# Optimization experiments

Measured on AMD Instinct MI355X. Metric: run time of the kernel, lower is better.

Reference implementation:

```python
import jax, jax.numpy as jnp
import numpy as np

B, S, H, E = 2, 4096, 2048, 8


def setup_inputs() -> dict:
    key = jax.random.key(0)
    k1, k2, k3 = jax.random.split(key, 3)
    x = jax.random.normal(k1, (B, S, H), dtype=jnp.float32)
    w_router = jax.random.normal(k2, (E, H), dtype=jnp.float32) * (1.0 / np.sqrt(H))
    # nn.Linear weight layout: [out_features, in_features] per expert -> [E, H, H]
    w_experts = jax.random.normal(k3, (E, H, H), dtype=jnp.float32) * (1.0 / np.sqrt(H))
    return {"x": x, "w_router": w_router, "w_experts": w_experts}


def reference(x, w_router, w_experts):
    # router logits: x @ W_r^T  -> [B, S, E]
    logits = jnp.einsum('bsh,eh->bse', x, w_router)
    idx = jnp.argmax(logits, axis=-1)  # [B, S] top-1 expert per token
    # dense all-expert outputs (matches original which evaluates every expert):
    # expert_e(x) = x @ W_e^T -> [B, S, E, H]
    all_out = jnp.einsum('bsh,efh->bsef', x, w_experts)
    # masked sum over one-hot mask == gather of the selected expert output
    out = jnp.take_along_axis(all_out, idx[:, :, None, None], axis=2)[:, :, 0, :]
    return out
```

## Files before the change

kernel.cpp:

```cpp
#include <hip/hip_runtime.h>
#include <hip/hip_bf16.h>
#include <cstdint>

#define T_TOK 8192
#define H_DIM 2048
#define N_EXP 8
#define FLAGBIT 0x80000000u

typedef __attribute__((ext_vector_type(4))) float f32x4;
typedef __attribute__((ext_vector_type(8))) short bf16x8;

__device__ __forceinline__ unsigned short f2bf(float f) {
  unsigned int u = __builtin_bit_cast(unsigned int, f);
  u += 0x7fffu + ((u >> 16) & 1u);
  return (unsigned short)(u >> 16);
}

#define GLL(SRC, DST) __builtin_amdgcn_global_load_lds( \
    (const __attribute__((address_space(1))) void*)(SRC), \
    (__attribute__((address_space(3))) void*)(DST), 16, 0, 0)

__global__ __launch_bounds__(256, 2) void k_conv(const float* __restrict__ we,
                                                 unsigned short* __restrict__ wb) {
  const size_t tix = ((size_t)blockIdx.x * 256 + threadIdx.x) * 8;
  const size_t stride = (size_t)2048 * 256 * 8;
  f32x4 v[16];
#pragma unroll
  for (int it = 0; it < 8; ++it) {
    v[2 * it]     = *reinterpret_cast<const f32x4*>(we + tix + (size_t)it * stride);
    v[2 * it + 1] = *reinterpret_cast<const f32x4*>(we + tix + (size_t)it * stride + 4);
  }
#pragma unroll
  for (int q = 0; q < 16; ++q) asm volatile("" : "+v"(v[q]));
#pragma unroll
  for (int it = 0; it < 8; ++it) {
    union { unsigned short h[8]; uint4 u; } r;
#pragma unroll
    for (int q = 0; q < 4; ++q) {
      r.h[q]     = f2bf(v[2 * it][q]);
      r.h[4 + q] = f2bf(v[2 * it + 1][q]);
    }
    *reinterpret_cast<uint4*>(wb + tix + (size_t)it * stride) = r.u;
  }
}

__global__ __launch_bounds__(256) void k_router(const float* __restrict__ x,
    const float* __restrict__ wr, unsigned short* __restrict__ xb,
    int* __restrict__ idx)
{
  __shared__ float swr[N_EXP * H_DIM];
#pragma unroll
  for (int i = 0; i < 16; ++i) {
    const int o = (threadIdx.x + i * 256) * 4;
    *reinterpret_cast<float4*>(&swr[o]) = *reinterpret_cast<const float4*>(&wr[o]);
  }
  __syncthreads();
  const int wv = threadIdx.x >> 6, lane = threadIdx.x & 63;
  const int t0 = (blockIdx.x * 4 + wv) * 4;
  float acc[4][N_EXP];
#pragma unroll
  for (int tt = 0; tt < 4; ++tt)
#pragma unroll
    for (int e = 0; e < N_EXP; ++e) acc[tt][e] = 0.f;
#pragma unroll
  for (int c = 0; c < H_DIM / 256; ++c) {
    const int h = c * 256 + lane * 4;
    float4 wvv[N_EXP];
#pragma unroll
    for (int e = 0; e < N_EXP; ++e)
      wvv[e] = *reinterpret_cast<const float4*>(&swr[e * H_DIM + h]);
#pragma unroll
    for (int tt = 0; tt < 4; ++tt) {
      const float4 xv = *reinterpret_cast<const float4*>(x + (size_t)(t0 + tt) * H_DIM + h);
      ushort4 bv;
      bv.x = f2bf(xv.x); bv.y = f2bf(xv.y); bv.z = f2bf(xv.z); bv.w = f2bf(xv.w);
      *reinterpret_cast<ushort4*>(xb + (size_t)(t0 + tt) * H_DIM + h) = bv;
#pragma unroll
      for (int e = 0; e < N_EXP; ++e) {
        acc[tt][e] = fmaf(xv.x, wvv[e].x, acc[tt][e]);
        acc[tt][e] = fmaf(xv.y, wvv[e].y, acc[tt][e]);
        acc[tt][e] = fmaf(xv.z, wvv[e].z, acc[tt][e]);
        acc[tt][e] = fmaf(xv.w, wvv[e].w, acc[tt][e]);
      }
    }
  }
#pragma unroll
  for (int off = 32; off >= 1; off >>= 1)
#pragma unroll
    for (int tt = 0; tt < 4; ++tt)
#pragma unroll
      for (int e = 0; e < N_EXP; ++e) acc[tt][e] += __shfl_xor(acc[tt][e], off, 64);
  if (lane == 0) {
#pragma unroll
    for (int tt = 0; tt < 4; ++tt) {
      float best = acc[tt][0]; int be = 0;
#pragma unroll
      for (int e = 1; e < N_EXP; ++e) if (acc[tt][e] > best) { best = acc[tt][e]; be = e; }
      idx[t0 + tt] = be;
    }
  }
}

__global__ __launch_bounds__(1024) void k_sort(const int* __restrict__ idx,
    int* __restrict__ tlist, int* __restrict__ estar, int* __restrict__ mlo,
    int* __restrict__ mhi, int* __restrict__ rpos, int* __restrict__ rtile,
    int* __restrict__ rtc)
{
  __shared__ int wc[N_EXP][128];
  __shared__ int wbase[N_EXP][128];
  __shared__ int sTot[N_EXP];
  __shared__ int off[N_EXP + 1];
  __shared__ int sE[32], sCnt[N_EXP], sBase[N_EXP];
  const int tid = threadIdx.x, w = tid >> 6, l = tid & 63;
  int myE[8];
#pragma unroll
  for (int j = 0; j < 8; ++j) {
    myE[j] = idx[j * 1024 + tid];
#pragma unroll
    for (int e = 0; e < N_EXP; ++e) {
      const unsigned long long bm = __ballot(myE[j] == e);
      if (l == e) wc[e][j * 16 + w] = __popcll(bm);
    }
  }
  __syncthreads();
  if (tid < N_EXP) {
    int s = 0;
    for (int k = 0; k < 128; ++k) { wbase[tid][k] = s; s += wc[tid][k]; }
    sTot[tid] = s;
  }
  __syncthreads();
  if (tid == 0) {
    off[0] = 0;
    for (int e = 0; e < N_EXP; ++e) off[e + 1] = off[e] + sTot[e];
  }
  __syncthreads();
#pragma unroll
  for (int j = 0; j < 8; ++j) {
    int rank = 0;
#pragma unroll
    for (int e = 0; e < N_EXP; ++e) {
      const unsigned long long bm = __ballot(myE[j] == e);
      if (myE[j] == e) rank = __popcll(bm & ((1ull << l) - 1ull));
    }
    tlist[off[myE[j]] + wbase[myE[j]][j * 16 + w] + rank] = j * 1024 + tid;
  }
  if (tid < 32) {
    const int lo = tid * 256, hi = lo + 256;
    int bl = -1, bE = 0, bLo = 0, bHi = 0;
#pragma unroll
    for (int e = 0; e < N_EXP; ++e) {
      const int a = off[e] > lo ? off[e] : lo;
      const int b = off[e + 1] < hi ? off[e + 1] : hi;
      if (b - a > bl) { bl = b - a; bE = e; bLo = a - lo; bHi = b - lo; }
    }
    sE[tid] = bE; estar[tid] = bE; mlo[tid] = bLo; mhi[tid] = bHi;
  }
  __syncthreads();
  if (tid < N_EXP) {
    int cnt = 0;
    for (int t = 0; t < 32; ++t) {
      if (sE[t] == tid) continue;
      const int lo = t * 256, hi = lo + 256;
      const int a = off[tid] > lo ? off[tid] : lo;
      const int b = off[tid + 1] < hi ? off[tid + 1] : hi;
      if (b > a) cnt += b - a;
    }
    sCnt[tid] = cnt;
  }
  __syncthreads();
  if (tid == 0) {
    int base = 0, ntile = 0;
    for (int e = 0; e < N_EXP; ++e) {
      sBase[e] = base;
      const int pt = (sCnt[e] + 127) >> 7;
      for (int k = 0; k < pt; ++k) rtile[ntile++] = e;
      base += pt << 7;
    }
    *rtc = ntile;
  }
  __syncthreads();
  if (tid < N_EXP && sCnt[tid] > 0) {
    int ptr = sBase[tid], firstp = -1;
    for (int t = 0; t < 32; ++t) {
      if (sE[t] == tid) continue;
      const int lo = t * 256, hi = lo + 256;
      const int a = off[tid] > lo ? off[tid] : lo;
      const int b = off[tid + 1] < hi ? off[tid + 1] : hi;
      for (int p = a; p < b; ++p) { if (firstp < 0) firstp = p; rpos[ptr++] = p; }
    }
    const int end = sBase[tid] + (((sCnt[tid] + 127) >> 7) << 7);
    for (; ptr < end; ++ptr) rpos[ptr] = (int)((unsigned)firstp | FLAGBIT);
  }
}

__global__ __launch_bounds__(256) void k_zero_min(const int* __restrict__ rpos,
    const int* __restrict__ tlist, const int* __restrict__ rtc,
    float* __restrict__ out)
{
  const int nslots = (*rtc) << 7;
  const float4 z = {0.f, 0.f, 0.f, 0.f};
  for (int s = blockIdx.x; s < nslots; s += 256) {
    const int ent = rpos[s];
    if ((unsigned)ent & FLAGBIT) continue;
    const int tok = tlist[ent];
    float* op = out + (size_t)tok * H_DIM;
    for (int i = threadIdx.x; i < H_DIM / 4; i += 256)
      reinterpret_cast<float4*>(op)[i] = z;
  }
}

__global__ __launch_bounds__(1024, 4) void k_gemm(const unsigned short* __restrict__ xb,
    const unsigned short* __restrict__ wb, const int* __restrict__ tlist,
    const int* __restrict__ estar, const int* __restrict__ mlo, const int* __restrict__ mhi,
    const int* __restrict__ rpos, const int* __restrict__ rtile, const int* __restrict__ rtc,
    float* __restrict__ out)
{
  __shared__ short lds[65536];
  const int bid = blockIdx.x;
  const int tid = threadIdx.x;
  const int l = tid & 63, wv = tid >> 6;
  const int l16 = l & 15, g16 = l >> 4;
  const char* LP = (const char*)lds;
  auto* LDS3 = (__attribute__((address_space(3))) char*)lds;

  if (bid < 256) {
    const int mt = (bid & 7) * 4 + ((bid >> 3) & 3);
    const int nt = bid >> 5;
    const int m0 = mt * 256, f0 = nt * 256;
    const int e = estar[mt], mLo = mlo[mt], mHi = mhi[mt];
    const int wm = wv >> 2, wn = wv & 3;

    const int ch = (g16 ^ ((l16 >> 1) & 3)) << 4;
    const int aRd = (wm * 64 + l16) * 64 + ch;
    const int bRd = 16384 + (wn * 64 + l16) * 64 + ch;

    const int csrc = (((l & 3) ^ ((l >> 3) & 3))) * 8;
    const int srow = l >> 2;
    const int tokA = tlist[m0 + wv * 16 + srow];
    const unsigned short* aS = xb + (size_t)tokA * H_DIM + csrc;
    const unsigned short* bS = wb + (size_t)e * H_DIM * H_DIM
                                  + (size_t)(f0 + wv * 16 + srow) * H_DIM + csrc;
    const int dA = wv * 1024;
    const int dB = 16384 + wv * 1024;

    f32x4 acc[4][4];
#pragma unroll
    for (int mf = 0; mf < 4; ++mf)
#pragma unroll
      for (int nf = 0; nf < 4; ++nf) acc[mf][nf] = (f32x4){0.f, 0.f, 0.f, 0.f};

    GLL(aS +  0, LDS3 + 0 * 32768 + dA);  GLL(bS +  0, LDS3 + 0 * 32768 + dB);
    GLL(aS + 32, LDS3 + 1 * 32768 + dA);  GLL(bS + 32, LDS3 + 1 * 32768 + dB);
    GLL(aS + 64, LDS3 + 2 * 32768 + dA);  GLL(bS + 64, LDS3 + 2 * 32768 + dB);
    asm volatile("s_waitcnt vmcnt(4)" ::: "memory");
    __builtin_amdgcn_sched_barrier(0);
    __builtin_amdgcn_s_barrier();
    __builtin_amdgcn_sched_barrier(0);

    for (int t = 0; t < 64; ++t) {
      const int buf  = (t & 3) * 32768;
      const int nbuf = ((t + 3) & 3) * 32768;
      const int kk   = ((t + 3) & 63) * 32;
      bf16x8 af[4], bf[4];
#pragma unroll
      for (int mf = 0; mf < 4; ++mf)
        af[mf] = *reinterpret_cast<const bf16x8*>(LP + buf + aRd + mf * 1024);
#pragma unroll
      for (int nf = 0; nf < 4; ++nf)
        bf[nf] = *reinterpret_cast<const bf16x8*>(LP + buf + bRd + nf * 1024);
      GLL(aS + kk, LDS3 + nbuf + dA);
      GLL(bS + kk, LDS3 + nbuf + dB);
      __builtin_amdgcn_s_setprio(1);
#pragma unroll
      for (int mf = 0; mf < 4; ++mf)
#pragma unroll
        for (int nf = 0; nf < 4; ++nf)
          acc[mf][nf] = __builtin_amdgcn_mfma_f32_16x16x32_bf16(af[mf], bf[nf], acc[mf][nf], 0, 0, 0);
      __builtin_amdgcn_s_setprio(0);
      asm volatile("s_waitcnt vmcnt(4)" ::: "memory");
      __builtin_amdgcn_sched_barrier(0);
      __builtin_amdgcn_s_barrier();
      __builtin_amdgcn_sched_barrier(0);
    }

#pragma unroll
    for (int mf = 0; mf < 4; ++mf) {
#pragma unroll
      for (int r = 0; r < 4; ++r) {
        const int row = wm * 64 + mf * 16 + g16 * 4 + r;
        if (row >= mLo && row < mHi) {
          const int t2 = tlist[m0 + row];
          float* op = out + (size_t)t2 * H_DIM + f0 + wn * 64 + l16;
#pragma unroll
          for (int nf = 0; nf < 4; ++nf) op[nf * 16] = acc[mf][nf][r];
        }
      }
    }
    return;
  }

  const int bid2 = bid - 256;
  const int bx = bid2 >> 4;
  if (bx >= *rtc) return;
  const int f0 = ((bid2 >> 1) & 7) * 256;
  const int kc = bid2 & 1;
  const int e = rtile[bx];
  const int wm = wv >> 2, wn = wv & 3;
  const int sw = l16 & 7;
  const int ch0 = ((0 + g16) ^ sw) << 4, ch1 = ((4 + g16) ^ sw) << 4;
  const int csrc8 = ((l & 7) ^ ((l >> 3) & 7)) * 8;
  const int srow8 = l >> 3;

  const unsigned short* aS;
  {
    const int ent = rpos[bx * 128 + wv * 8 + srow8];
    const int tok = tlist[ent & 0x7fffffff];
    aS = xb + (size_t)tok * H_DIM + csrc8;
  }
  const unsigned short* bS0 = wb + (size_t)e * H_DIM * H_DIM
                                 + (size_t)(f0 + wv * 8 + srow8) * H_DIM + csrc8;
  const unsigned short* bS1 = bS0 + (size_t)128 * H_DIM;

  f32x4 acc[2][4];
#pragma unroll
  for (int mf = 0; mf < 2; ++mf)
#pragma unroll
    for (int nf = 0; nf < 4; ++nf) acc[mf][nf] = (f32x4){0.f, 0.f, 0.f, 0.f};

  for (int it = 0; it < 16; ++it) {
    const int kk = kc * 1024 + it * 64;
    __syncthreads();
    GLL(aS + kk, LDS3 + wv * 1024);
    GLL(bS0 + kk, LDS3 + 16384 + wv * 1024);
    GLL(bS1 + kk, LDS3 + 16384 + 16384 + wv * 1024);
    __syncthreads();
    bf16x8 af[2][2];
#pragma unroll
    for (int mf = 0; mf < 2; ++mf) {
      af[mf][0] = *reinterpret_cast<const bf16x8*>(LP + (wm * 32 + mf * 16 + l16) * 128 + ch0);
      af[mf][1] = *reinterpret_cast<const bf16x8*>(LP + (wm * 32 + mf * 16 + l16) * 128 + ch1);
    }
#pragma unroll
    for (int nf = 0; nf < 4; ++nf) {
      const bf16x8 b0 = *reinterpret_cast<const bf16x8*>(LP + 16384 + (wn * 64 + nf * 16 + l16) * 128 + ch0);
      const bf16x8 b1 = *reinterpret_cast<const bf16x8*>(LP + 16384 + (wn * 64 + nf * 16 + l16) * 128 + ch1);
#pragma unroll
      for (int mf = 0; mf < 2; ++mf) {
        acc[mf][nf] = __builtin_amdgcn_mfma_f32_16x16x32_bf16(af[mf][0], b0, acc[mf][nf], 0, 0, 0);
        acc[mf][nf] = __builtin_amdgcn_mfma_f32_16x16x32_bf16(af[mf][1], b1, acc[mf][nf], 0, 0, 0);
      }
    }
  }
#pragma unroll
  for (int mf = 0; mf < 2; ++mf) {
#pragma unroll
    for (int r = 0; r < 4; ++r) {
      const int row = wm * 32 + mf * 16 + g16 * 4 + r;
      const int ent = rpos[bx * 128 + row];
      if (!((unsigned)ent & FLAGBIT)) {
        const int tok = tlist[ent];
        float* op = out + (size_t)tok * H_DIM + f0 + wn * 64 + l16;
#pragma unroll
        for (int nf = 0; nf < 4; ++nf) atomicAdd(op + nf * 16, acc[mf][nf][r]);
      }
    }
  }
}

extern "C" void kernel_launch(void* const* d_in, const int* in_sizes, int n_in,
                              void* d_out, int out_size, void* d_ws, size_t ws_size,
                              hipStream_t stream) {
  const float* x  = (const float*)d_in[0];
  const float* wr = (const float*)d_in[1];
  const float* we = (const float*)d_in[2];
  float* out = (float*)d_out;

  char* p = (char*)d_ws;
  unsigned short* xb = (unsigned short*)p; p += (size_t)T_TOK * H_DIM * 2;
  unsigned short* wb = (unsigned short*)p; p += (size_t)N_EXP * H_DIM * H_DIM * 2;
  int* idx    = (int*)p; p += T_TOK * 4;
  int* tlist  = (int*)p; p += T_TOK * 4;
  int* rpos   = (int*)p; p += T_TOK * 4;
  int* estar  = (int*)p; p += 32 * 4;
  int* mlo    = (int*)p; p += 32 * 4;
  int* mhi    = (int*)p; p += 32 * 4;
  int* rtile  = (int*)p; p += 64 * 4;
  int* rtc    = (int*)p; p += 64;

  k_conv<<<2048, 256, 0, stream>>>(we, wb);
  k_router<<<512, 256, 0, stream>>>(x, wr, xb, idx);
  k_sort<<<1, 1024, 0, stream>>>(idx, tlist, estar, mlo, mhi, rpos, rtile, rtc);
  k_zero_min<<<256, 256, 0, stream>>>(rpos, tlist, rtc, out);
  k_gemm<<<256 + 1024, 1024, 0, stream>>>(xb, wb, tlist, estar, mlo, mhi, rpos, rtile, rtc, out);
}
```

Before: 189.2 us.

## Fuse expert weight bf16 conversion into GEMM by loading fp32 weights into LDS

Removes the separate k_conv pass that converted all 8 expert weight matrices to bf16. The GEMM now streams fp32 weights directly into LDS and converts them to bf16 with v_cvt_pk_bf16_f32 right before the MFMAs. LDS buffering changes from four stages to three larger stages, and the tail path halves its k-step. This saves a full read and write of the weight tensor, but the GEMM now reads twice the bytes for B, and each weight tile may be fetched by several M-tiles while carrying extra conversion ALU in the inner loop.

```diff
diff --git a/kernel.cpp b/kernel.cpp
--- a/kernel.cpp
+++ b/kernel.cpp
@@ -16,33 +16,15 @@
   return (unsigned short)(u >> 16);
 }
 
+__device__ __forceinline__ unsigned cvtpk(float lo, float hi) {
+  unsigned r;
+  asm("v_cvt_pk_bf16_f32 %0, %1, %2" : "=v"(r) : "v"(lo), "v"(hi));
+  return r;
+}
+
 #define GLL(SRC, DST) __builtin_amdgcn_global_load_lds( \
     (const __attribute__((address_space(1))) void*)(SRC), \
     (__attribute__((address_space(3))) void*)(DST), 16, 0, 0)
-
-__global__ __launch_bounds__(256, 2) void k_conv(const float* __restrict__ we,
-                                                 unsigned short* __restrict__ wb) {
-  const size_t tix = ((size_t)blockIdx.x * 256 + threadIdx.x) * 8;
-  const size_t stride = (size_t)2048 * 256 * 8;
-  f32x4 v[16];
-#pragma unroll
-  for (int it = 0; it < 8; ++it) {
-    v[2 * it]     = *reinterpret_cast<const f32x4*>(we + tix + (size_t)it * stride);
-    v[2 * it + 1] = *reinterpret_cast<const f32x4*>(we + tix + (size_t)it * stride + 4);
-  }
-#pragma unroll
-  for (int q = 0; q < 16; ++q) asm volatile("" : "+v"(v[q]));
-#pragma unroll
-  for (int it = 0; it < 8; ++it) {
-    union { unsigned short h[8]; uint4 u; } r;
-#pragma unroll
-    for (int q = 0; q < 4; ++q) {
-      r.h[q]     = f2bf(v[2 * it][q]);
-      r.h[4 + q] = f2bf(v[2 * it + 1][q]);
-    }
-    *reinterpret_cast<uint4*>(wb + tix + (size_t)it * stride) = r.u;
-  }
-}
 
 __global__ __launch_bounds__(256) void k_router(const float* __restrict__ x,
     const float* __restrict__ wr, unsigned short* __restrict__ xb,
@@ -210,12 +192,12 @@
 }
 
 __global__ __launch_bounds__(1024, 4) void k_gemm(const unsigned short* __restrict__ xb,
-    const unsigned short* __restrict__ wb, const int* __restrict__ tlist,
+    const float* __restrict__ we, const int* __restrict__ tlist,
     const int* __restrict__ estar, const int* __restrict__ mlo, const int* __restrict__ mhi,
     const int* __restrict__ rpos, const int* __restrict__ rtile, const int* __restrict__ rtc,
     float* __restrict__ out)
 {
-  __shared__ short lds[65536];
+  __shared__ short lds[73728];
   const int bid = blockIdx.x;
   const int tid = threadIdx.x;
   const int l = tid & 63, wv = tid >> 6;
@@ -230,18 +212,22 @@
     const int e = estar[mt], mLo = mlo[mt], mHi = mhi[mt];
     const int wm = wv >> 2, wn = wv & 3;
 
-    const int ch = (g16 ^ ((l16 >> 1) & 3)) << 4;
-    const int aRd = (wm * 64 + l16) * 64 + ch;
-    const int bRd = 16384 + (wn * 64 + l16) * 64 + ch;
-
-    const int csrc = (((l & 3) ^ ((l >> 3) & 3))) * 8;
-    const int srow = l >> 2;
-    const int tokA = tlist[m0 + wv * 16 + srow];
-    const unsigned short* aS = xb + (size_t)tokA * H_DIM + csrc;
-    const unsigned short* bS = wb + (size_t)e * H_DIM * H_DIM
-                                  + (size_t)(f0 + wv * 16 + srow) * H_DIM + csrc;
+    const int chA = (g16 ^ ((l16 >> 1) & 3)) << 4;
+    const int aRd = (wm * 64 + l16) * 64 + chA;
+    const int chB0 = ((2 * g16 + 0) ^ (l16 & 7)) << 4;
+    const int chB1 = ((2 * g16 + 1) ^ (l16 & 7)) << 4;
+    const int bRd = 16384 + (wn * 64 + l16) * 128;
+
+    const int csrcA = ((l & 3) ^ ((l >> 3) & 3)) * 8;
+    const int tokA = tlist[m0 + wv * 16 + (l >> 2)];
+    const unsigned short* aS = xb + (size_t)tokA * H_DIM + csrcA;
     const int dA = wv * 1024;
-    const int dB = 16384 + wv * 1024;
+    const int csrcB = ((l & 7) ^ ((l >> 3) & 7)) * 4;
+    const float* bS0 = we + (size_t)e * H_DIM * H_DIM
+                          + (size_t)(f0 + wv * 8 + (l >> 3)) * H_DIM + csrcB;
+    const float* bS1 = bS0 + (size_t)128 * H_DIM;
+    const int dB0 = 16384 + wv * 1024;
+    const int dB1 = 16384 + 16384 + wv * 1024;
 
     f32x4 acc[4][4];
 #pragma unroll
@@ -249,38 +235,43 @@
 #pragma unroll
       for (int nf = 0; nf < 4; ++nf) acc[mf][nf] = (f32x4){0.f, 0.f, 0.f, 0.f};
 
-    GLL(aS +  0, LDS3 + 0 * 32768 + dA);  GLL(bS +  0, LDS3 + 0 * 32768 + dB);
-    GLL(aS + 32, LDS3 + 1 * 32768 + dA);  GLL(bS + 32, LDS3 + 1 * 32768 + dB);
-    GLL(aS + 64, LDS3 + 2 * 32768 + dA);  GLL(bS + 64, LDS3 + 2 * 32768 + dB);
-    asm volatile("s_waitcnt vmcnt(4)" ::: "memory");
+    GLL(aS +  0, LDS3 + 0 + dA);  GLL(bS0 +  0, LDS3 + 0 + dB0);  GLL(bS1 +  0, LDS3 + 0 + dB1);
+    GLL(aS + 32, LDS3 + 49152 + dA);  GLL(bS0 + 32, LDS3 + 49152 + dB0);  GLL(bS1 + 32, LDS3 + 49152 + dB1);
+    asm volatile("s_waitcnt vmcnt(3)" ::: "memory");
     __builtin_amdgcn_sched_barrier(0);
     __builtin_amdgcn_s_barrier();
     __builtin_amdgcn_sched_barrier(0);
 
+    int cur = 0;
     for (int t = 0; t < 64; ++t) {
-      const int buf  = (t & 3) * 32768;
-      const int nbuf = ((t + 3) & 3) * 32768;
-      const int kk   = ((t + 3) & 63) * 32;
-      bf16x8 af[4], bf[4];
+      int nb = cur + 2; if (nb >= 3) nb -= 3;
+      const int buf = cur * 49152, nbuf = nb * 49152;
+      const int kk = ((t + 2) & 63) * 32;
+      bf16x8 af[4];
 #pragma unroll
       for (int mf = 0; mf < 4; ++mf)
         af[mf] = *reinterpret_cast<const bf16x8*>(LP + buf + aRd + mf * 1024);
-#pragma unroll
-      for (int nf = 0; nf < 4; ++nf)
-        bf[nf] = *reinterpret_cast<const bf16x8*>(LP + buf + bRd + nf * 1024);
       GLL(aS + kk, LDS3 + nbuf + dA);
-      GLL(bS + kk, LDS3 + nbuf + dB);
+      GLL(bS0 + kk, LDS3 + nbuf + dB0);
+      GLL(bS1 + kk, LDS3 + nbuf + dB1);
       __builtin_amdgcn_s_setprio(1);
 #pragma unroll
-      for (int mf = 0; mf < 4; ++mf)
-#pragma unroll
-        for (int nf = 0; nf < 4; ++nf)
-          acc[mf][nf] = __builtin_amdgcn_mfma_f32_16x16x32_bf16(af[mf], bf[nf], acc[mf][nf], 0, 0, 0);
+      for (int nf = 0; nf < 4; ++nf) {
+        const f32x4 lo = *reinterpret_cast<const f32x4*>(LP + buf + bRd + nf * 2048 + chB0);
+        const f32x4 hi = *reinterpret_cast<const f32x4*>(LP + buf + bRd + nf * 2048 + chB1);
+        union { unsigned u[4]; bf16x8 v; } bfu;
+        bfu.u[0] = cvtpk(lo[0], lo[1]); bfu.u[1] = cvtpk(lo[2], lo[3]);
+        bfu.u[2] = cvtpk(hi[0], hi[1]); bfu.u[3] = cvtpk(hi[2], hi[3]);
+#pragma unroll
+        for (int mf = 0; mf < 4; ++mf)
+          acc[mf][nf] = __builtin_amdgcn_mfma_f32_16x16x32_bf16(af[mf], bfu.v, acc[mf][nf], 0, 0, 0);
+      }
       __builtin_amdgcn_s_setprio(0);
-      asm volatile("s_waitcnt vmcnt(4)" ::: "memory");
+      asm volatile("s_waitcnt vmcnt(3)" ::: "memory");
       __builtin_amdgcn_sched_barrier(0);
       __builtin_amdgcn_s_barrier();
       __builtin_amdgcn_sched_barrier(0);
+      cur = (cur + 1 == 3) ? 0 : cur + 1;
     }
 
 #pragma unroll
@@ -306,20 +297,22 @@
   const int kc = bid2 & 1;
   const int e = rtile[bx];
   const int wm = wv >> 2, wn = wv & 3;
-  const int sw = l16 & 7;
-  const int ch0 = ((0 + g16) ^ sw) << 4, ch1 = ((4 + g16) ^ sw) << 4;
-  const int csrc8 = ((l & 7) ^ ((l >> 3) & 7)) * 8;
-  const int srow8 = l >> 3;
-
-  const unsigned short* aS;
-  {
-    const int ent = rpos[bx * 128 + wv * 8 + srow8];
+
+  const int chA = (g16 ^ ((l16 >> 1) & 3)) << 4;
+  const int chB0 = ((2 * g16 + 0) ^ (l16 & 7)) << 4;
+  const int chB1 = ((2 * g16 + 1) ^ (l16 & 7)) << 4;
+  const int csrcA = ((l & 3) ^ ((l >> 3) & 3)) * 8;
+  const int csrcB = ((l & 7) ^ ((l >> 3) & 7)) * 4;
+
+  const unsigned short* aS = nullptr;
+  if (wv < 8) {
+    const int ent = rpos[bx * 128 + wv * 16 + (l >> 2)];
     const int tok = tlist[ent & 0x7fffffff];
-    aS = xb + (size_t)tok * H_DIM + csrc8;
-  }
-  const unsigned short* bS0 = wb + (size_t)e * H_DIM * H_DIM
-                                 + (size_t)(f0 + wv * 8 + srow8) * H_DIM + csrc8;
-  const unsigned short* bS1 = bS0 + (size_t)128 * H_DIM;
+    aS = xb + (size_t)tok * H_DIM + csrcA;
+  }
+  const float* bS0 = we + (size_t)e * H_DIM * H_DIM
+                        + (size_t)(f0 + wv * 8 + (l >> 3)) * H_DIM + csrcB;
+  const float* bS1 = bS0 + (size_t)128 * H_DIM;
 
   f32x4 acc[2][4];
 #pragma unroll
@@ -327,28 +320,28 @@
 #pragma unroll
     for (int nf = 0; nf < 4; ++nf) acc[mf][nf] = (f32x4){0.f, 0.f, 0.f, 0.f};
 
-  for (int it = 0; it < 16; ++it) {
-    const int kk = kc * 1024 + it * 64;
+  for (int it = 0; it < 32; ++it) {
+    const int kk = kc * 1024 + it * 32;
     __syncthreads();
-    GLL(aS + kk, LDS3 + wv * 1024);
-    GLL(bS0 + kk, LDS3 + 16384 + wv * 1024);
-    GLL(bS1 + kk, LDS3 + 16384 + 16384 + wv * 1024);
+    if (wv < 8) GLL(aS + kk, LDS3 + wv * 1024);
+    GLL(bS0 + kk, LDS3 + 8192 + wv * 1024);
+    GLL(bS1 + kk, LDS3 + 8192 + 16384 + wv * 1024);
     __syncthreads();
-    bf16x8 af[2][2];
-#pragma unroll
-    for (int mf = 0; mf < 2; ++mf) {
-      af[mf][0] = *reinterpret_cast<const bf16x8*>(LP + (wm * 32 + mf * 16 + l16) * 128 + ch0);
-      af[mf][1] = *reinterpret_cast<const bf16x8*>(LP + (wm * 32 + mf * 16 + l16) * 128 + ch1);
-    }
+    bf16x8 af[2];
+#pragma unroll
+    for (int mf = 0; mf < 2; ++mf)
+      af[mf] = *reinterpret_cast<const bf16x8*>(LP + (wm * 32 + mf * 16 + l16) * 64 + chA);
 #pragma unroll
     for (int nf = 0; nf < 4; ++nf) {
-      const bf16x8 b0 = *reinterpret_cast<const bf16x8*>(LP + 16384 + (wn * 64 + nf * 16 + l16) * 128 + ch0);
-      const bf16x8 b1 = *reinterpret_cast<const bf16x8*>(LP + 16384 + (wn * 64 + nf * 16 + l16) * 128 + ch1);
-#pragma unroll
-      for (int mf = 0; mf < 2; ++mf) {
-        acc[mf][nf] = __builtin_amdgcn_mfma_f32_16x16x32_bf16(af[mf][0], b0, acc[mf][nf], 0, 0, 0);
-        acc[mf][nf] = __builtin_amdgcn_mfma_f32_16x16x32_bf16(af[mf][1], b1, acc[mf][nf], 0, 0, 0);
-      }
+      const int bRd = 8192 + (wn * 64 + nf * 16 + l16) * 128;
+      const f32x4 lo = *reinterpret_cast<const f32x4*>(LP + bRd + chB0);
+      const f32x4 hi = *reinterpret_cast<const f32x4*>(LP + bRd + chB1);
+      union { unsigned u[4]; bf16x8 v; } bfu;
+      bfu.u[0] = cvtpk(lo[0], lo[1]); bfu.u[1] = cvtpk(lo[2], lo[3]);
+      bfu.u[2] = cvtpk(hi[0], hi[1]); bfu.u[3] = cvtpk(hi[2], hi[3]);
+#pragma unroll
+      for (int mf = 0; mf < 2; ++mf)
+        acc[mf][nf] = __builtin_amdgcn_mfma_f32_16x16x32_bf16(af[mf], bfu.v, acc[mf][nf], 0, 0, 0);
     }
   }
 #pragma unroll
@@ -377,7 +370,6 @@
 
   char* p = (char*)d_ws;
   unsigned short* xb = (unsigned short*)p; p += (size_t)T_TOK * H_DIM * 2;
-  unsigned short* wb = (unsigned short*)p; p += (size_t)N_EXP * H_DIM * H_DIM * 2;
   int* idx    = (int*)p; p += T_TOK * 4;
   int* tlist  = (int*)p; p += T_TOK * 4;
   int* rpos   = (int*)p; p += T_TOK * 4;
@@ -387,9 +379,8 @@
   int* rtile  = (int*)p; p += 64 * 4;
   int* rtc    = (int*)p; p += 64;
 
-  k_conv<<<2048, 256, 0, stream>>>(we, wb);
   k_router<<<512, 256, 0, stream>>>(x, wr, xb, idx);
   k_sort<<<1, 1024, 0, stream>>>(idx, tlist, estar, mlo, mhi, rpos, rtile, rtc);
   k_zero_min<<<256, 256, 0, stream>>>(rpos, tlist, rtc, out);
-  k_gemm<<<256 + 1024, 1024, 0, stream>>>(xb, wb, tlist, estar, mlo, mhi, rpos, rtile, rtc, out);
-}
+  k_gemm<<<256 + 1024, 1024, 0, stream>>>(xb, we, tlist, estar, mlo, mhi, rpos, rtile, rtc, out);
+}
```

Measured after the change: 193.0 us. Within noise of the previous version (+2.0%).
